# Performance work log

Hardware: AMD Instinct MI355X
Metric: run time of the kernel (lower is better)

The kernel has to match this reference:

```python
import jax, jax.numpy as jnp
import numpy as np
from jax import lax

SIGMA = 0.03
ALPHA = 1.0
MASK_VALUE = -1e-8
SAMPLE_NUM = 131072  # static stand-in for the dynamic edge-pixel count


def _sobel_edges(images):
    # images: [n,3,h,w]; torch code uses only channel 0 when c==3
    kx = jnp.array([[-1., 0., 1.], [-2., 0., 2.], [-1., 0., 1.]], dtype=images.dtype).reshape(1, 1, 3, 3)
    ky = jnp.array([[1., 2., 1.], [0., 0., 0.], [-1., -2., -1.]], dtype=images.dtype).reshape(1, 1, 3, 3)
    x = images[:, :1]
    dn = ('NCHW', 'OIHW', 'NCHW')
    gx = lax.conv_general_dilated(x, kx, (1, 1), 'VALID', dimension_numbers=dn)
    gy = lax.conv_general_dilated(x, ky, (1, 1), 'VALID', dimension_numbers=dn)
    edges = jnp.sqrt(gx * gx + gy * gy)
    thetas = jnp.arctan2(gy, gx)
    pad = ((0, 0), (0, 0), (1, 1), (1, 1))
    return jnp.pad(edges, pad), jnp.pad(thetas, pad)


def _per_image_loss(inp, tgt, msk, edge, theta, ra, rd, rp, h, w):
    # all flat vectors of length P = h*w; ra:[S], rd:[4,S], rp:[2S]
    # --- edge-guided sampling ---
    emax = edge.max()
    emask = edge >= 0.1 * emax
    minlen = jnp.maximum(emask.sum(), 1)
    edge_idx = jnp.argsort(jnp.logical_not(emask), stable=True)  # edge pixels first
    anchor_pix = edge_idx[ra % minlen]
    theta_a = theta[anchor_pix]
    row_a = anchor_pix // w
    col_a = anchor_pix % w
    sign = jnp.array([-1., -1., 1., 1.], dtype=inp.dtype)[:, None]
    dist = (rd.astype(inp.dtype) + 2.0) * sign  # magnitudes in [2,31)
    col4 = jnp.clip(col_a[None, :] + jnp.round(dist * jnp.cos(theta_a)[None, :]).astype(jnp.int32), 0, w - 1)
    row4 = jnp.clip(row_a[None, :] + jnp.round(dist * jnp.sin(theta_a)[None, :]).astype(jnp.int32), 0, h - 1)
    pix = row4 * w + col4  # sub2ind, [4,S]
    A = jnp.concatenate([pix[0], pix[1], pix[2]])  # [3S]
    B = jnp.concatenate([pix[1], pix[2], pix[3]])
    # --- random sampling among valid (targets > threshold) pixels ---
    vmask = tgt > MASK_VALUE
    nvalid = jnp.maximum(vmask.sum(), 1)
    vidx = jnp.argsort(jnp.logical_not(vmask), stable=True)
    sh = rp % nvalid
    rA = vidx[sh[0::2]]
    rB = vidx[sh[1::2]]
    Ai = jnp.concatenate([A, rA])  # [4S]
    Bi = jnp.concatenate([B, rB])
    iA, iB = inp[Ai], inp[Bi]
    tA, tB = tgt[Ai], tgt[Bi]
    mA, mB = msk[Ai], msk[Bi]
    # --- ranking loss ---
    ratio = (tA + 1e-6) / (tB + 1e-6)
    hi = 1.0 + SIGMA
    lo = 1.0 / hi
    mask_eq = (ratio < hi) & (ratio > lo)
    labels = jnp.where(ratio >= hi, 1.0, 0.0) + jnp.where(ratio <= lo, -1.0, 0.0)
    cm = mA * mB
    equal_loss = (iA - iB) ** 2 * mask_eq.astype(inp.dtype) * cm
    unequal_loss = jnp.log1p(jnp.exp((iB - iA) * labels)) * (~mask_eq).astype(inp.dtype) * cm
    return ALPHA * equal_loss.mean() + unequal_loss.mean()


def reference(inputs, targets, images, rand_anchor, rand_dist, rand_perm):
    n, c, h, w = targets.shape
    masks = (targets > MASK_VALUE).astype(targets.dtype)
    edges, thetas = _sobel_edges(images)
    P = h * w
    flat = lambda x: x.reshape(n, P)
    per_img = lambda i, t, m, e, th, ra, rd, rp: _per_image_loss(i, t, m, e, th, ra, rd, rp, h, w)
    losses = jax.vmap(per_img)(flat(inputs), flat(targets), flat(masks), flat(edges), flat(thetas),
                               rand_anchor, rand_dist, rand_perm)
    return (losses.sum() / n).astype(jnp.float32)


def setup_inputs() -> dict:
    key = jax.random.key(0)
    k1, k2, k3, k4, k5, k6 = jax.random.split(key, 6)
    n, h, w = 4, 768, 1024
    P = h * w
    S = SAMPLE_NUM
    return {
        'inputs': jax.random.normal(k1, (n, 1, h, w), dtype=jnp.float32),
        'targets': jax.random.uniform(k2, (n, 1, h, w), dtype=jnp.float32),
        'images': jax.random.uniform(k3, (n, 3, h, w), dtype=jnp.float32),
        'rand_anchor': jax.random.randint(k4, (n, S), 0, P, dtype=jnp.int32),
        'rand_dist': jax.random.randint(k5, (n, 4, S), 0, 29, dtype=jnp.int32),
        'rand_perm': jax.random.randint(k6, (n, 2 * S), 0, P, dtype=jnp.int32),
    }
```

## Files before the change

kernel.cpp:

```cpp
#include <hip/hip_runtime.h>
#include <math.h>

#define W 1024
#define H 768
#define PIX (W*H)
#define NIMG 4
#define SNUM 131072
#define BPI 3072
#define NBP (NIMG*BPI)
#define UPB 12
#define NBC 1024
#define MASKV (-1e-8f)

__device__ __forceinline__ void sobel_g(const float* __restrict__ img, int y, int x,
                                        float& gx, float& gy) {
    const float* r0 = img + (y - 1) * W + x;
    const float* r1 = r0 + W;
    const float* r2 = r1 + W;
    float a00 = r0[-1], a01 = r0[0], a02 = r0[1];
    float a10 = r1[-1],              a12 = r1[1];
    float a20 = r2[-1], a21 = r2[0], a22 = r2[1];
    gx = (a02 - a00) + 2.f * (a12 - a10) + (a22 - a20);
    gy = (a00 - a20) + 2.f * (a01 - a21) + (a02 - a22);
}

__global__ void prep_kernel(const float* __restrict__ inputs,
                            const float* __restrict__ targets,
                            const float* __restrict__ images,
                            float2* __restrict__ pairIT,
                            int* __restrict__ compVSeg,
                            float* __restrict__ blockmax,
                            int* __restrict__ blkV) {
    int b = blockIdx.x, t = threadIdx.x;
    int i = b / BPI, unit = b - i * BPI;
    int gp = unit * 256 + t;
    int y = gp >> 10, x = gp & (W - 1);
    const float* img = images + (size_t)i * 3 * PIX;
    float e = 0.f;
    if (y >= 1 && y <= H - 2 && x >= 1 && x <= W - 2) {
        float gx, gy;
        sobel_g(img, y, x, gx, gy);
        e = sqrtf(gx * gx + gy * gy);
    }
    size_t off = (size_t)i * PIX + gp;
    float inv = inputs[off], tgv = targets[off];
    pairIT[off] = make_float2(inv, tgv);

    int lane = t & 63, w = t >> 6;
    bool v = tgv > MASKV;
    unsigned long long mV = __ballot(v);
    __shared__ float sm[256];
    __shared__ int sW[4];
    if (lane == 0) sW[w] = __popcll(mV);
    sm[t] = e;
    __syncthreads();
    int base = 0;
    for (int q = 0; q < w; q++) base += sW[q];
    if (t == 0) blkV[b] = sW[0] + sW[1] + sW[2] + sW[3];
    if (v) compVSeg[off - t + base + __popcll(mV & ((1ull << lane) - 1ull))] = gp;
    for (int o = 128; o > 0; o >>= 1) {
        if (t < o) sm[t] = fmaxf(sm[t], sm[t + o]);
        __syncthreads();
    }
    if (t == 0) blockmax[b] = sm[0];
}

__global__ void compact_kernel(const float* __restrict__ images,
                               const float* __restrict__ blockmax,
                               const int* __restrict__ blkV,
                               float2* __restrict__ anchorSeg,
                               int* __restrict__ cntE,
                               int* __restrict__ SVg,
                               int* __restrict__ vtotG) {
    int blk = blockIdx.x, t = threadIdx.x;
    int i = blk >> 8, bb = blk & 255;
    const float* img = images + (size_t)i * 3 * PIX;
    int lane = t & 63, w = t >> 6;
    unsigned long long lm = (1ull << lane) - 1ull;

    __shared__ float sRed[256];
    __shared__ int sW2[4];
    const float* bm = blockmax + i * BPI;
    float mx = 0.f;
#pragma unroll
    for (int k = 0; k < 12; k++) mx = fmaxf(mx, bm[t + k * 256]);
    sRed[t] = mx;
    __syncthreads();
    for (int o = 128; o > 0; o >>= 1) {
        if (t < o) sRed[t] = fmaxf(sRed[t], sRed[t + o]);
        __syncthreads();
    }
    float thr = 0.1f * sRed[0];

    for (int k = 0; k < UPB; k++) {
        int unit = bb * UPB + k;
        int gp = unit * 256 + t;
        int y = gp >> 10, x = gp & (W - 1);
        float e = 0.f, gx = 0.f, gy = 0.f;
        bool inner = (y >= 1 && y <= H - 2 && x >= 1 && x <= W - 2);
        if (inner) { sobel_g(img, y, x, gx, gy); e = sqrtf(gx * gx + gy * gy); }
        bool isE = (e >= thr);
        unsigned long long mE = __ballot(isE);
        __syncthreads();
        if (lane == 0) sW2[w] = __popcll(mE);
        __syncthreads();
        int base = 0;
        for (int q = 0; q < w; q++) base += sW2[q];
        if (t == 0) cntE[i * BPI + unit] = sW2[0] + sW2[1] + sW2[2] + sW2[3];
        if (isE) {
            float th = inner ? atan2f(gy, gx) : 0.f;
            anchorSeg[(size_t)i * PIX + unit * 256 + base + __popcll(mE & lm)] =
                make_float2(__int_as_float(gp), th);
        }
    }

    if (bb == 0) {
        __syncthreads();
        __shared__ int sT[256];
        const int* bv = blkV + i * BPI;
        int loc[12]; int tot = 0;
#pragma unroll
        for (int k = 0; k < 12; k++) { loc[k] = bv[t * 12 + k]; tot += loc[k]; }
        sT[t] = tot;
        __syncthreads();
        for (int o = 1; o < 256; o <<= 1) {
            int v = (t >= o) ? sT[t - o] : 0;
            __syncthreads();
            sT[t] += v;
            __syncthreads();
        }
        int run = sT[t] - tot;
        int* sv = SVg + i * BPI;
#pragma unroll
        for (int k = 0; k < 12; k++) { sv[t * 12 + k] = run; run += loc[k]; }
        if (t == 255) vtotG[i] = sT[255];
    }
}

__device__ __forceinline__ void pair_term(float2 a, float2 b, float& eqs, float& uns) {
    float cm = ((a.y > MASKV) ? 1.f : 0.f) * ((b.y > MASKV) ? 1.f : 0.f);
    float ratio = (a.y + 1e-6f) / (b.y + 1e-6f);
    const float HIv = 1.03f;
    const float LOv = (float)(1.0 / 1.03);
    bool eq = (ratio < HIv) && (ratio > LOv);
    if (eq) {
        float d = a.x - b.x;
        eqs += d * d * cm;
    } else {
        float label = ((ratio >= HIv) ? 1.f : 0.f) + ((ratio <= LOv) ? -1.f : 0.f);
        uns += log1pf(expf((b.x - a.x) * label)) * cm;
    }
}

__global__ void loss_kernel(const float2* __restrict__ pairIT,
                            const float2* __restrict__ anchorSeg,
                            const int* __restrict__ compVSeg,
                            const int* __restrict__ cntE,
                            const int* __restrict__ SVg,
                            const int* __restrict__ vtotG,
                            const int* __restrict__ ra, const int* __restrict__ rd,
                            const int* __restrict__ rp,
                            float2* __restrict__ partials) {
    int i = blockIdx.y, t = threadIdx.x;
    __shared__ int S[BPI];
    __shared__ int sT[256];
    {
        const int* ce = cntE + i * BPI;
        int loc[12]; int tot = 0;
#pragma unroll
        for (int k = 0; k < 12; k++) { loc[k] = ce[t * 12 + k]; tot += loc[k]; }
        sT[t] = tot;
        __syncthreads();
        for (int o = 1; o < 256; o <<= 1) {
            int v = (t >= o) ? sT[t - o] : 0;
            __syncthreads();
            sT[t] += v;
            __syncthreads();
        }
        int run = sT[t] - tot;
#pragma unroll
        for (int k = 0; k < 12; k++) { S[t * 12 + k] = run; run += loc[k]; }
        __syncthreads();
    }
    int eT = sT[255];
    int vT = vtotG[i];
    int nval = (vT > 0) ? vT : 1;

    int s = blockIdx.x * 256 + t;
    const float2* pIT = pairIT + (size_t)i * PIX;

    int j = ra[(size_t)i * SNUM + s] % eT;
    int lo = 0, hi = BPI - 1;
#pragma unroll
    for (int k = 0; k < 12; k++) {
        int mid = (lo + hi + 1) >> 1;
        if (S[mid] <= j) lo = mid; else hi = mid - 1;
    }
    float2 ac = anchorSeg[(size_t)i * PIX + lo * 256 + (j - S[lo])];
    int anchor = __float_as_int(ac.x);
    float sv = sinf(ac.y), cv = cosf(ac.y);
    int row_a = anchor >> 10, col_a = anchor & (W - 1);

    int pix4[4];
#pragma unroll
    for (int k = 0; k < 4; k++) {
        int r = rd[((size_t)i * 4 + k) * SNUM + s];
        float dist = ((float)r + 2.0f) * ((k < 2) ? -1.f : 1.f);
        int cc = col_a + (int)rintf(dist * cv);
        int rr = row_a + (int)rintf(dist * sv);
        cc = min(max(cc, 0), W - 1);
        rr = min(max(rr, 0), H - 1);
        pix4[k] = (rr << 10) | cc;
    }
    int2 rr2 = *(const int2*)(rp + (size_t)i * 2 * SNUM + 2 * s);
    int r0 = rr2.x % nval, r1 = rr2.y % nval;
    int A, B;
    if ((vT == PIX) || (vT == 0)) {
        A = r0; B = r1;
    } else {
        const int* SV = SVg + i * BPI;
        int lo2 = 0, hi2 = BPI - 1;
        int lo3 = 0, hi3 = BPI - 1;
#pragma unroll
        for (int k = 0; k < 12; k++) {
            int m2 = (lo2 + hi2 + 1) >> 1;
            if (SV[m2] <= r0) lo2 = m2; else hi2 = m2 - 1;
            int m3 = (lo3 + hi3 + 1) >> 1;
            if (SV[m3] <= r1) lo3 = m3; else hi3 = m3 - 1;
        }
        A = compVSeg[(size_t)i * PIX + lo2 * 256 + (r0 - SV[lo2])];
        B = compVSeg[(size_t)i * PIX + lo3 * 256 + (r1 - SV[lo3])];
    }

    float2 a0 = pIT[pix4[0]], a1 = pIT[pix4[1]], a2 = pIT[pix4[2]], a3 = pIT[pix4[3]];
    float2 b0 = pIT[A], b1 = pIT[B];
    float eqs = 0.f, uns = 0.f;
    pair_term(a0, a1, eqs, uns);
    pair_term(a1, a2, eqs, uns);
    pair_term(a2, a3, eqs, uns);
    pair_term(b0, b1, eqs, uns);

    __shared__ float sEq[256], sUn[256];
    sEq[t] = eqs; sUn[t] = uns;
    __syncthreads();
    for (int o = 128; o > 0; o >>= 1) {
        if (t < o) { sEq[t] += sEq[t + o]; sUn[t] += sUn[t + o]; }
        __syncthreads();
    }
    if (t == 0)
        partials[i * 512 + blockIdx.x] = make_float2(sEq[0], sUn[0]);
}

__global__ void final_kernel(const float2* __restrict__ partials, float* __restrict__ out) {
    int t = threadIdx.x;
    double acc = 0.0;
#pragma unroll
    for (int k = 0; k < 8; k++) {
        float2 p = partials[t + k * 256];
        acc += (double)p.x + (double)p.y;
    }
    __shared__ double sm[256];
    sm[t] = acc;
    __syncthreads();
    for (int o = 128; o > 0; o >>= 1) {
        if (t < o) sm[t] += sm[t + o];
        __syncthreads();
    }
    if (t == 0) {
        double denom = 4.0 * (double)SNUM;
        out[0] = (float)(sm[0] / denom / (double)NIMG);
    }
}

extern "C" void kernel_launch(void* const* d_in, const int* in_sizes, int n_in,
                              void* d_out, int out_size, void* d_ws, size_t ws_size,
                              hipStream_t stream) {
    const float* inputs  = (const float*)d_in[0];
    const float* targets = (const float*)d_in[1];
    const float* images  = (const float*)d_in[2];
    const int* ra = (const int*)d_in[3];
    const int* rd = (const int*)d_in[4];
    const int* rp = (const int*)d_in[5];
    float* out = (float*)d_out;

    char* ws = (char*)d_ws;
    int*      vtotG    = (int*)ws;
    float*    blockmax = (float*)(ws + 1024);
    int*      blkV     = (int*)(ws + 50176);
    int*      cntE     = (int*)(ws + 99328);
    int*      SVg      = (int*)(ws + 148480);
    float2*   partials = (float2*)(ws + 197632);
    float2*   pairIT   = (float2*)(ws + 1048576);
    float2*   anchorSeg= (float2*)(ws + 26214400);
    int*      compVSeg = (int*)(ws + 51380224);

    prep_kernel<<<NBP, 256, 0, stream>>>(inputs, targets, images,
                                         pairIT, compVSeg, blockmax, blkV);
    compact_kernel<<<NBC, 256, 0, stream>>>(images, blockmax, blkV,
                                            anchorSeg, cntE, SVg, vtotG);
    loss_kernel<<<dim3(512, NIMG), 256, 0, stream>>>(pairIT, anchorSeg, compVSeg,
                                                     cntE, SVg, vtotG,
                                                     ra, rd, rp, partials);
    final_kernel<<<1, 256, 0, stream>>>(partials, out);
}
```

Measured before the change: 180.1 us.

## Store input/target pairs as half2 and move valid-pixel compaction into compact kernel

The packed input/target buffer is stored as half2 instead of float2, halving its write traffic in prep and the gather traffic in the loss kernel. Valid-pixel compaction moves out of prep into compact_kernel, which first sums the valid counts and skips compaction entirely when every pixel is valid. The fp16 rounding of targets can change the ratio comparisons and the mask threshold test (tiny targets may round to zero), so results may drift from the fp32 reference.

```diff
diff --git a/kernel.cpp b/kernel.cpp
--- a/kernel.cpp
+++ b/kernel.cpp
@@ -1,4 +1,5 @@
 #include <hip/hip_runtime.h>
+#include <hip/hip_fp16.h>
 #include <math.h>
 
 #define W 1024
@@ -27,8 +28,7 @@
 __global__ void prep_kernel(const float* __restrict__ inputs,
                             const float* __restrict__ targets,
                             const float* __restrict__ images,
-                            float2* __restrict__ pairIT,
-                            int* __restrict__ compVSeg,
+                            __half2* __restrict__ pairIT,
                             float* __restrict__ blockmax,
                             int* __restrict__ blkV) {
     int b = blockIdx.x, t = threadIdx.x;
@@ -44,20 +44,19 @@
     }
     size_t off = (size_t)i * PIX + gp;
     float inv = inputs[off], tgv = targets[off];
-    pairIT[off] = make_float2(inv, tgv);
+    __half2 h;
+    h.x = __float2half_rn(inv);
+    h.y = __float2half_rn(tgv);
+    pairIT[off] = h;
 
     int lane = t & 63, w = t >> 6;
-    bool v = tgv > MASKV;
-    unsigned long long mV = __ballot(v);
+    unsigned long long mV = __ballot(tgv > MASKV);
     __shared__ float sm[256];
     __shared__ int sW[4];
     if (lane == 0) sW[w] = __popcll(mV);
     sm[t] = e;
     __syncthreads();
-    int base = 0;
-    for (int q = 0; q < w; q++) base += sW[q];
     if (t == 0) blkV[b] = sW[0] + sW[1] + sW[2] + sW[3];
-    if (v) compVSeg[off - t + base + __popcll(mV & ((1ull << lane) - 1ull))] = gp;
     for (int o = 128; o > 0; o >>= 1) {
         if (t < o) sm[t] = fmaxf(sm[t], sm[t + o]);
         __syncthreads();
@@ -66,9 +65,11 @@
 }
 
 __global__ void compact_kernel(const float* __restrict__ images,
+                               const float* __restrict__ targets,
                                const float* __restrict__ blockmax,
                                const int* __restrict__ blkV,
                                float2* __restrict__ anchorSeg,
+                               int* __restrict__ compVSeg,
                                int* __restrict__ cntE,
                                int* __restrict__ SVg,
                                int* __restrict__ vtotG) {
@@ -79,18 +80,21 @@
     unsigned long long lm = (1ull << lane) - 1ull;
 
     __shared__ float sRed[256];
+    __shared__ int sRedI[256];
     __shared__ int sW2[4];
     const float* bm = blockmax + i * BPI;
-    float mx = 0.f;
-#pragma unroll
-    for (int k = 0; k < 12; k++) mx = fmaxf(mx, bm[t + k * 256]);
-    sRed[t] = mx;
+    const int* bv = blkV + i * BPI;
+    float mx = 0.f; int sv = 0;
+#pragma unroll
+    for (int k = 0; k < 12; k++) { mx = fmaxf(mx, bm[t + k * 256]); sv += bv[t + k * 256]; }
+    sRed[t] = mx; sRedI[t] = sv;
     __syncthreads();
     for (int o = 128; o > 0; o >>= 1) {
-        if (t < o) sRed[t] = fmaxf(sRed[t], sRed[t + o]);
+        if (t < o) { sRed[t] = fmaxf(sRed[t], sRed[t + o]); sRedI[t] += sRedI[t + o]; }
         __syncthreads();
     }
     float thr = 0.1f * sRed[0];
+    int vtotR = sRedI[0];
 
     for (int k = 0; k < UPB; k++) {
         int unit = bb * UPB + k;
@@ -114,10 +118,24 @@
         }
     }
 
+    if (vtotR < PIX) {
+        for (int k = 0; k < UPB; k++) {
+            int unit = bb * UPB + k;
+            int gp = unit * 256 + t;
+            bool v = targets[(size_t)i * PIX + gp] > MASKV;
+            unsigned long long mV = __ballot(v);
+            __syncthreads();
+            if (lane == 0) sW2[w] = __popcll(mV);
+            __syncthreads();
+            int base = 0;
+            for (int q = 0; q < w; q++) base += sW2[q];
+            if (v) compVSeg[(size_t)i * PIX + unit * 256 + base + __popcll(mV & lm)] = gp;
+        }
+    }
+
     if (bb == 0) {
         __syncthreads();
         __shared__ int sT[256];
-        const int* bv = blkV + i * BPI;
         int loc[12]; int tot = 0;
 #pragma unroll
         for (int k = 0; k < 12; k++) { loc[k] = bv[t * 12 + k]; tot += loc[k]; }
@@ -130,9 +148,9 @@
             __syncthreads();
         }
         int run = sT[t] - tot;
-        int* sv = SVg + i * BPI;
-#pragma unroll
-        for (int k = 0; k < 12; k++) { sv[t * 12 + k] = run; run += loc[k]; }
+        int* svp = SVg + i * BPI;
+#pragma unroll
+        for (int k = 0; k < 12; k++) { svp[t * 12 + k] = run; run += loc[k]; }
         if (t == 255) vtotG[i] = sT[255];
     }
 }
@@ -152,7 +170,11 @@
     }
 }
 
-__global__ void loss_kernel(const float2* __restrict__ pairIT,
+__device__ __forceinline__ float2 h2f(__half2 h) {
+    return make_float2(__half2float(h.x), __half2float(h.y));
+}
+
+__global__ void loss_kernel(const __half2* __restrict__ pairIT,
                             const float2* __restrict__ anchorSeg,
                             const int* __restrict__ compVSeg,
                             const int* __restrict__ cntE,
@@ -187,7 +209,7 @@
     int nval = (vT > 0) ? vT : 1;
 
     int s = blockIdx.x * 256 + t;
-    const float2* pIT = pairIT + (size_t)i * PIX;
+    const __half2* pIT = pairIT + (size_t)i * PIX;
 
     int j = ra[(size_t)i * SNUM + s] % eT;
     int lo = 0, hi = BPI - 1;
@@ -232,8 +254,9 @@
         B = compVSeg[(size_t)i * PIX + lo3 * 256 + (r1 - SV[lo3])];
     }
 
-    float2 a0 = pIT[pix4[0]], a1 = pIT[pix4[1]], a2 = pIT[pix4[2]], a3 = pIT[pix4[3]];
-    float2 b0 = pIT[A], b1 = pIT[B];
+    float2 a0 = h2f(pIT[pix4[0]]), a1 = h2f(pIT[pix4[1]]);
+    float2 a2 = h2f(pIT[pix4[2]]), a3 = h2f(pIT[pix4[3]]);
+    float2 b0 = h2f(pIT[A]), b1 = h2f(pIT[B]);
     float eqs = 0.f, uns = 0.f;
     pair_term(a0, a1, eqs, uns);
     pair_term(a1, a2, eqs, uns);
@@ -290,14 +313,14 @@
     int*      cntE     = (int*)(ws + 99328);
     int*      SVg      = (int*)(ws + 148480);
     float2*   partials = (float2*)(ws + 197632);
-    float2*   pairIT   = (float2*)(ws + 1048576);
-    float2*   anchorSeg= (float2*)(ws + 26214400);
-    int*      compVSeg = (int*)(ws + 51380224);
+    __half2*  pairIT   = (__half2*)(ws + 1048576);
+    float2*   anchorSeg= (float2*)(ws + 14680064);
+    int*      compVSeg = (int*)(ws + 39845888);
 
     prep_kernel<<<NBP, 256, 0, stream>>>(inputs, targets, images,
-                                         pairIT, compVSeg, blockmax, blkV);
-    compact_kernel<<<NBC, 256, 0, stream>>>(images, blockmax, blkV,
-                                            anchorSeg, cntE, SVg, vtotG);
+                                         pairIT, blockmax, blkV);
+    compact_kernel<<<NBC, 256, 0, stream>>>(images, targets, blockmax, blkV,
+                                            anchorSeg, compVSeg, cntE, SVg, vtotG);
     loss_kernel<<<dim3(512, NIMG), 256, 0, stream>>>(pairIT, anchorSeg, compVSeg,
                                                      cntE, SVg, vtotG,
                                                      ra, rd, rp, partials);
```

After: 168.4 us. 6.5% less time.
